# Performance work log

Measured on AMD Instinct MI355X. Metric: run time of the kernel, lower is better.

The kernel has to match this reference:

```python
import jax, jax.numpy as jnp
import numpy as np

B, S, DIM, DA = 64, 4096, 256, 64
NEG = -1e30

def setup_inputs() -> dict:
    key = jax.random.key(0)
    k1, k2, k3, k4 = jax.random.split(key, 4)
    h = jax.random.normal(k1, (B, S, DIM), dtype=jnp.float32)
    mask = jax.random.randint(k2, (B, S), 0, 2).astype(jnp.bool_)
    # xavier_uniform with gain=1.414 as in the torch module
    lim_a = 1.414 * np.sqrt(6.0 / (DIM + DA))
    lim_b = 1.414 * np.sqrt(6.0 / (DA + 1))
    a = jax.random.uniform(k3, (DIM, DA), minval=-lim_a, maxval=lim_a, dtype=jnp.float32)
    b = jax.random.uniform(k4, (DA, 1), minval=-lim_b, maxval=lim_b, dtype=jnp.float32)
    return {"h": h, "mask": mask, "a": a, "b": b}

def reference(h, mask, a, b):
    # e: (B, S) additive-attention logits
    e = jnp.einsum('bsk,ko->bs', jnp.tanh(jnp.einsum('bsd,dk->bsk', h, a)), b)
    e = e + mask.astype(e.dtype) * NEG  # True == padding -> -1e30
    attn = jax.nn.softmax(e, axis=1)    # softmax over seq dim
    # weighted sum over seq: (B, DIM)
    return jnp.einsum('bs,bsd->bd', attn, h)
```

## Files before the change

kernel.cpp:

```cpp
#include <hip/hip_runtime.h>
#include <hip/hip_bf16.h>

#define B_      64
#define S_      4096
#define DIM_    256
#define DA_     64
#define NEG_    (-1e30f)
#define CHUNKS_ 16
#define ROWS_   256
#define LDH_    264
#define PSTR_   260

typedef _Float16 half8 __attribute__((ext_vector_type(8)));
typedef float float4v __attribute__((ext_vector_type(4)));

__device__ __forceinline__ float tanh_fast(float x) {
    float e = __expf(2.0f * x);
    return 1.0f - 2.0f * __builtin_amdgcn_rcpf(e + 1.0f);
}

__global__ __launch_bounds__(256) void prep_kernel(
    const float* __restrict__ a, const void* __restrict__ mask,
    _Float16* __restrict__ at_sw, int* __restrict__ flag)
{
    int idx = blockIdx.x * 256 + threadIdx.x;
    int j    = idx & 7;
    int lane = (idx >> 3) & 63;
    int kbnt = idx >> 9;
    int kb   = kbnt & 7;
    int nt   = kbnt >> 3;
    int d  = kb * 32 + (lane >> 4) * 8 + j;
    int kf = nt * 16 + (lane & 15);
    at_sw[idx] = (_Float16)a[d * DA_ + kf];

    if (blockIdx.x == 0) {
        __shared__ int anynz;
        if (threadIdx.x == 0) anynz = 0;
        __syncthreads();
        const unsigned char* mb = (const unsigned char*)mask;
        int base = threadIdx.x * 4;
        int v = mb[base + 1] | mb[base + 2] | mb[base + 3];
        if (v) atomicOr(&anynz, 1);
        __syncthreads();
        if (threadIdx.x == 0) *flag = (anynz == 0) ? 1 : 0;
    }
}

__global__ __launch_bounds__(256, 2) void fused_kernel(
    const float* __restrict__ h, const _Float16* __restrict__ at_sw,
    const float* __restrict__ bvec, const void* __restrict__ mask,
    const int* __restrict__ flag, float* __restrict__ part)
{
    __shared__ _Float16 asw[16384];
    __shared__ _Float16 hf[64 * LDH_];

    const int t    = threadIdx.x;
    const int wave = t >> 6;
    const int lane = t & 63;
    const int quad = lane >> 4;
    const int nrow = lane & 15;
    const bool int32enc = (*flag != 0);

    {
        const uint4* g = (const uint4*)at_sw;
        uint4* l = (uint4*)asw;
        #pragma unroll
        for (int i = 0; i < 8; ++i) l[i * 256 + t] = g[i * 256 + t];
    }

    float4 bq[4];
    #pragma unroll
    for (int nt = 0; nt < 4; ++nt)
        bq[nt] = *(const float4*)(bvec + nt * 16 + quad * 4);

    const int cg = blockIdx.x;
    const int b  = cg >> 4;
    const int c  = cg & 15;
    const long long crow = (long long)b * S_ + c * ROWS_;
    const long long row0 = crow + wave * 16 + nrow;

    int mv0, mv1, mv2, mv3;
    if (int32enc) {
        const int* mi = (const int*)mask + row0;
        mv0 = mi[0]; mv1 = mi[64]; mv2 = mi[128]; mv3 = mi[192];
    } else {
        const unsigned char* mb = (const unsigned char*)mask + row0;
        mv0 = mb[0]; mv1 = mb[64]; mv2 = mb[128]; mv3 = mb[192];
    }

    __syncthreads();

    const float* wbase = h + (crow + wave * 16) * DIM_;
    float acc0 = 0.f, acc1 = 0.f, acc2 = 0.f, acc3 = 0.f;
    float m_w = NEG_, l_w = 0.f;

    float4 pf[16];

    #pragma unroll
    for (int i = 0; i < 16; ++i)
        pf[i] = *(const float4*)(wbase + (size_t)i * DIM_ + lane * 4);
    #pragma unroll
    for (int i = 0; i < 16; ++i) {
        union { _Float16 hh[4]; unsigned long long u; } pk;
        pk.hh[0] = (_Float16)pf[i].x; pk.hh[1] = (_Float16)pf[i].y;
        pk.hh[2] = (_Float16)pf[i].z; pk.hh[3] = (_Float16)pf[i].w;
        *(unsigned long long*)&hf[(wave * 16 + i) * LDH_ + lane * 4] = pk.u;
    }

    auto body = [&](int tile, int mv) {
        if (tile < 3) {
            const float* nb = wbase + (size_t)(tile + 1) * 64 * DIM_;
            #pragma unroll
            for (int i = 0; i < 16; ++i)
                pf[i] = *(const float4*)(nb + (size_t)i * DIM_ + lane * 4);
        }

        const _Float16* hrow_l = &hf[(wave * 16 + nrow) * LDH_];
        float4v accm[4];
        #pragma unroll
        for (int nt = 0; nt < 4; ++nt) accm[nt] = (float4v){0.f, 0.f, 0.f, 0.f};
        #pragma unroll
        for (int kb = 0; kb < 8; ++kb) {
            half8 bf = *(const half8*)(hrow_l + kb * 32 + quad * 8);
            #pragma unroll
            for (int nt = 0; nt < 4; ++nt) {
                half8 af = *(const half8*)&asw[((nt * 8 + kb) * 64 + lane) * 8];
                accm[nt] = __builtin_amdgcn_mfma_f32_16x16x32_f16(af, bf, accm[nt], 0, 0, 0);
            }
        }

        float p = 0.f;
        #pragma unroll
        for (int nt = 0; nt < 4; ++nt) {
            p += tanh_fast(accm[nt][0]) * bq[nt].x;
            p += tanh_fast(accm[nt][1]) * bq[nt].y;
            p += tanh_fast(accm[nt][2]) * bq[nt].z;
            p += tanh_fast(accm[nt][3]) * bq[nt].w;
        }
        p += __shfl_xor(p, 16);
        p += __shfl_xor(p, 32);

        float ev = mv ? NEG_ : p;
        float mx = ev;
        mx = fmaxf(mx, __shfl_xor(mx, 1));
        mx = fmaxf(mx, __shfl_xor(mx, 2));
        mx = fmaxf(mx, __shfl_xor(mx, 4));
        mx = fmaxf(mx, __shfl_xor(mx, 8));
        float m_new = fmaxf(m_w, mx);
        float rs  = __expf(m_w - m_new);
        float w_s = __expf(ev - m_new);
        float sm = w_s;
        sm += __shfl_xor(sm, 1);
        sm += __shfl_xor(sm, 2);
        sm += __shfl_xor(sm, 4);
        sm += __shfl_xor(sm, 8);
        l_w = l_w * rs + sm;
        m_w = m_new;
        acc0 *= rs; acc1 *= rs; acc2 *= rs; acc3 *= rs;

        #pragma unroll
        for (int s = 0; s < 16; ++s) {
            float wv = __shfl(w_s, s);
            union { ushort4 u; _Float16 hh[4]; } pk;
            pk.u = *(const ushort4*)((const unsigned short*)
                       &hf[(wave * 16 + s) * LDH_ + lane * 4]);
            acc0 = fmaf(wv, (float)pk.hh[0], acc0);
            acc1 = fmaf(wv, (float)pk.hh[1], acc1);
            acc2 = fmaf(wv, (float)pk.hh[2], acc2);
            acc3 = fmaf(wv, (float)pk.hh[3], acc3);
        }

        if (tile < 3) {
            #pragma unroll
            for (int i = 0; i < 16; ++i) {
                union { _Float16 hh[4]; unsigned long long u; } pk;
                pk.hh[0] = (_Float16)pf[i].x; pk.hh[1] = (_Float16)pf[i].y;
                pk.hh[2] = (_Float16)pf[i].z; pk.hh[3] = (_Float16)pf[i].w;
                *(unsigned long long*)&hf[(wave * 16 + i) * LDH_ + lane * 4] = pk.u;
            }
        }
    };
    body(0, mv0); body(1, mv1); body(2, mv2); body(3, mv3);

    float* pc = part + (size_t)(cg * 4 + wave) * PSTR_;
    *(float4*)(pc + 4 + lane * 4) = make_float4(acc0, acc1, acc2, acc3);
    if (lane == 0) { pc[0] = m_w; pc[1] = l_w; }
}

__global__ __launch_bounds__(256) void merge_kernel(
    const float* __restrict__ part, float* __restrict__ out)
{
    const int b = blockIdx.x;
    const int t = threadIdx.x;
    const float* pb = part + (size_t)b * 64 * PSTR_;
    float M = NEG_;
    #pragma unroll
    for (int i = 0; i < 64; ++i) M = fmaxf(M, pb[i * PSTR_]);
    float L = 0.f, o = 0.f;
    #pragma unroll
    for (int i = 0; i < 64; ++i) {
        float sc = __expf(pb[i * PSTR_] - M);
        L += pb[i * PSTR_ + 1] * sc;
        o += pb[i * PSTR_ + 4 + t] * sc;
    }
    out[b * DIM_ + t] = o / L;
}

extern "C" void kernel_launch(void* const* d_in, const int* in_sizes, int n_in,
                              void* d_out, int out_size, void* d_ws, size_t ws_size,
                              hipStream_t stream) {
    const float* h    = (const float*)d_in[0];
    const void*  mask = d_in[1];
    const float* a    = (const float*)d_in[2];
    const float* bvec = (const float*)d_in[3];
    float* out = (float*)d_out;

    char* ws = (char*)d_ws;
    _Float16* at_sw = (_Float16*)ws;
    int* flag       = (int*)(ws + 32768);
    float* part     = (float*)(ws + 36864);

    prep_kernel<<<64, 256, 0, stream>>>(a, mask, at_sw, flag);
    fused_kernel<<<B_ * CHUNKS_, 256, 0, stream>>>(h, at_sw, bvec, mask, flag, part);
    merge_kernel<<<B_, 256, 0, stream>>>(part, out);
}
```

Before: 430.1 us.

## Split sequence into 64-row tiles per block and load h directly into MFMA fragments

Each block now handles a single 64-row tile, replacing four tiles with a software-prefetched register pipeline, so the grid grows from 1024 to 4096 blocks. Each lane loads its own MFMA B-fragment from global memory, converts it to fp16, and writes it to LDS for the weighted-sum pass, which removes the separate cooperative staging. This drops the online-softmax rescaling across tiles and the large prefetch register array, trading them for more parallelism. The cost is four times as many partials for the merge kernel, a longer serial merge loop per batch, and less coalesced strided per-lane global loads.

```diff
diff --git a/kernel.cpp b/kernel.cpp
--- a/kernel.cpp
+++ b/kernel.cpp
@@ -6,10 +6,9 @@
 #define DIM_    256
 #define DA_     64
 #define NEG_    (-1e30f)
-#define CHUNKS_ 16
-#define ROWS_   256
+#define NTILE_  64
 #define LDH_    264
-#define PSTR_   260
+#define PSTR_   264
 
 typedef _Float16 half8 __attribute__((ext_vector_type(8)));
 typedef float float4v __attribute__((ext_vector_type(4)));
@@ -73,118 +72,86 @@
     for (int nt = 0; nt < 4; ++nt)
         bq[nt] = *(const float4*)(bvec + nt * 16 + quad * 4);
 
-    const int cg = blockIdx.x;
-    const int b  = cg >> 4;
-    const int c  = cg & 15;
-    const long long crow = (long long)b * S_ + c * ROWS_;
-    const long long row0 = crow + wave * 16 + nrow;
+    const int bid = blockIdx.x;
+    const long long rowg = ((long long)(bid >> 6) * S_) + (bid & 63) * 64
+                         + wave * 16 + nrow;
+    const float* hp = h + rowg * DIM_ + quad * 8;
 
-    int mv0, mv1, mv2, mv3;
-    if (int32enc) {
-        const int* mi = (const int*)mask + row0;
-        mv0 = mi[0]; mv1 = mi[64]; mv2 = mi[128]; mv3 = mi[192];
-    } else {
-        const unsigned char* mb = (const unsigned char*)mask + row0;
-        mv0 = mb[0]; mv1 = mb[64]; mv2 = mb[128]; mv3 = mb[192];
-    }
+    int mv = int32enc ? ((const int*)mask)[rowg]
+                      : (int)((const unsigned char*)mask)[rowg];
 
     __syncthreads();
 
-    const float* wbase = h + (crow + wave * 16) * DIM_;
-    float acc0 = 0.f, acc1 = 0.f, acc2 = 0.f, acc3 = 0.f;
-    float m_w = NEG_, l_w = 0.f;
-
-    float4 pf[16];
+    const int lrow = wave * 16 + nrow;
+    float4v accm[4];
+    #pragma unroll
+    for (int nt = 0; nt < 4; ++nt) accm[nt] = (float4v){0.f, 0.f, 0.f, 0.f};
 
     #pragma unroll
-    for (int i = 0; i < 16; ++i)
-        pf[i] = *(const float4*)(wbase + (size_t)i * DIM_ + lane * 4);
-    #pragma unroll
-    for (int i = 0; i < 16; ++i) {
-        union { _Float16 hh[4]; unsigned long long u; } pk;
-        pk.hh[0] = (_Float16)pf[i].x; pk.hh[1] = (_Float16)pf[i].y;
-        pk.hh[2] = (_Float16)pf[i].z; pk.hh[3] = (_Float16)pf[i].w;
-        *(unsigned long long*)&hf[(wave * 16 + i) * LDH_ + lane * 4] = pk.u;
-    }
-
-    auto body = [&](int tile, int mv) {
-        if (tile < 3) {
-            const float* nb = wbase + (size_t)(tile + 1) * 64 * DIM_;
-            #pragma unroll
-            for (int i = 0; i < 16; ++i)
-                pf[i] = *(const float4*)(nb + (size_t)i * DIM_ + lane * 4);
+    for (int kh = 0; kh < 2; ++kh) {
+        float4 hv[8];
+        #pragma unroll
+        for (int i = 0; i < 8; ++i) {
+            int kb = kh * 4 + (i >> 1);
+            hv[i] = *(const float4*)(hp + kb * 32 + (i & 1) * 4);
         }
-
-        const _Float16* hrow_l = &hf[(wave * 16 + nrow) * LDH_];
-        float4v accm[4];
         #pragma unroll
-        for (int nt = 0; nt < 4; ++nt) accm[nt] = (float4v){0.f, 0.f, 0.f, 0.f};
-        #pragma unroll
-        for (int kb = 0; kb < 8; ++kb) {
-            half8 bf = *(const half8*)(hrow_l + kb * 32 + quad * 8);
+        for (int k = 0; k < 4; ++k) {
+            int kb = kh * 4 + k;
+            union { _Float16 hh[8]; half8 v; } pk;
+            pk.hh[0] = (_Float16)hv[2 * k].x;     pk.hh[1] = (_Float16)hv[2 * k].y;
+            pk.hh[2] = (_Float16)hv[2 * k].z;     pk.hh[3] = (_Float16)hv[2 * k].w;
+            pk.hh[4] = (_Float16)hv[2 * k + 1].x; pk.hh[5] = (_Float16)hv[2 * k + 1].y;
+            pk.hh[6] = (_Float16)hv[2 * k + 1].z; pk.hh[7] = (_Float16)hv[2 * k + 1].w;
+            *(half8*)&hf[lrow * LDH_ + kb * 32 + quad * 8] = pk.v;
             #pragma unroll
             for (int nt = 0; nt < 4; ++nt) {
                 half8 af = *(const half8*)&asw[((nt * 8 + kb) * 64 + lane) * 8];
-                accm[nt] = __builtin_amdgcn_mfma_f32_16x16x32_f16(af, bf, accm[nt], 0, 0, 0);
+                accm[nt] = __builtin_amdgcn_mfma_f32_16x16x32_f16(af, pk.v, accm[nt], 0, 0, 0);
             }
         }
+    }
 
-        float p = 0.f;
-        #pragma unroll
-        for (int nt = 0; nt < 4; ++nt) {
-            p += tanh_fast(accm[nt][0]) * bq[nt].x;
-            p += tanh_fast(accm[nt][1]) * bq[nt].y;
-            p += tanh_fast(accm[nt][2]) * bq[nt].z;
-            p += tanh_fast(accm[nt][3]) * bq[nt].w;
-        }
-        p += __shfl_xor(p, 16);
-        p += __shfl_xor(p, 32);
+    float p = 0.f;
+    #pragma unroll
+    for (int nt = 0; nt < 4; ++nt) {
+        p += tanh_fast(accm[nt][0]) * bq[nt].x;
+        p += tanh_fast(accm[nt][1]) * bq[nt].y;
+        p += tanh_fast(accm[nt][2]) * bq[nt].z;
+        p += tanh_fast(accm[nt][3]) * bq[nt].w;
+    }
+    p += __shfl_xor(p, 16);
+    p += __shfl_xor(p, 32);
 
-        float ev = mv ? NEG_ : p;
-        float mx = ev;
-        mx = fmaxf(mx, __shfl_xor(mx, 1));
-        mx = fmaxf(mx, __shfl_xor(mx, 2));
-        mx = fmaxf(mx, __shfl_xor(mx, 4));
-        mx = fmaxf(mx, __shfl_xor(mx, 8));
-        float m_new = fmaxf(m_w, mx);
-        float rs  = __expf(m_w - m_new);
-        float w_s = __expf(ev - m_new);
-        float sm = w_s;
-        sm += __shfl_xor(sm, 1);
-        sm += __shfl_xor(sm, 2);
-        sm += __shfl_xor(sm, 4);
-        sm += __shfl_xor(sm, 8);
-        l_w = l_w * rs + sm;
-        m_w = m_new;
-        acc0 *= rs; acc1 *= rs; acc2 *= rs; acc3 *= rs;
+    float ev = mv ? NEG_ : p;
+    float mx = ev;
+    mx = fmaxf(mx, __shfl_xor(mx, 1));
+    mx = fmaxf(mx, __shfl_xor(mx, 2));
+    mx = fmaxf(mx, __shfl_xor(mx, 4));
+    mx = fmaxf(mx, __shfl_xor(mx, 8));
+    float w_s = __expf(ev - mx);
+    float sm = w_s;
+    sm += __shfl_xor(sm, 1);
+    sm += __shfl_xor(sm, 2);
+    sm += __shfl_xor(sm, 4);
+    sm += __shfl_xor(sm, 8);
 
-        #pragma unroll
-        for (int s = 0; s < 16; ++s) {
-            float wv = __shfl(w_s, s);
-            union { ushort4 u; _Float16 hh[4]; } pk;
-            pk.u = *(const ushort4*)((const unsigned short*)
-                       &hf[(wave * 16 + s) * LDH_ + lane * 4]);
-            acc0 = fmaf(wv, (float)pk.hh[0], acc0);
-            acc1 = fmaf(wv, (float)pk.hh[1], acc1);
-            acc2 = fmaf(wv, (float)pk.hh[2], acc2);
-            acc3 = fmaf(wv, (float)pk.hh[3], acc3);
-        }
+    float acc0 = 0.f, acc1 = 0.f, acc2 = 0.f, acc3 = 0.f;
+    #pragma unroll
+    for (int s = 0; s < 16; ++s) {
+        float wv = __shfl(w_s, s);
+        union { ushort4 u; _Float16 hh[4]; } pk;
+        pk.u = *(const ushort4*)((const unsigned short*)
+                   &hf[(wave * 16 + s) * LDH_ + lane * 4]);
+        acc0 = fmaf(wv, (float)pk.hh[0], acc0);
+        acc1 = fmaf(wv, (float)pk.hh[1], acc1);
+        acc2 = fmaf(wv, (float)pk.hh[2], acc2);
+        acc3 = fmaf(wv, (float)pk.hh[3], acc3);
+    }
 
-        if (tile < 3) {
-            #pragma unroll
-            for (int i = 0; i < 16; ++i) {
-                union { _Float16 hh[4]; unsigned long long u; } pk;
-                pk.hh[0] = (_Float16)pf[i].x; pk.hh[1] = (_Float16)pf[i].y;
-                pk.hh[2] = (_Float16)pf[i].z; pk.hh[3] = (_Float16)pf[i].w;
-                *(unsigned long long*)&hf[(wave * 16 + i) * LDH_ + lane * 4] = pk.u;
-            }
-        }
-    };
-    body(0, mv0); body(1, mv1); body(2, mv2); body(3, mv3);
-
-    float* pc = part + (size_t)(cg * 4 + wave) * PSTR_;
+    float* pc = part + (size_t)(bid * 4 + wave) * PSTR_;
     *(float4*)(pc + 4 + lane * 4) = make_float4(acc0, acc1, acc2, acc3);
-    if (lane == 0) { pc[0] = m_w; pc[1] = l_w; }
+    if (lane == 0) { pc[0] = mx; pc[1] = sm; }
 }
 
 __global__ __launch_bounds__(256) void merge_kernel(
@@ -192,13 +159,13 @@
 {
     const int b = blockIdx.x;
     const int t = threadIdx.x;
-    const float* pb = part + (size_t)b * 64 * PSTR_;
+    const float* pb = part + (size_t)b * 256 * PSTR_;
     float M = NEG_;
-    #pragma unroll
-    for (int i = 0; i < 64; ++i) M = fmaxf(M, pb[i * PSTR_]);
+    #pragma unroll 8
+    for (int i = 0; i < 256; ++i) M = fmaxf(M, pb[i * PSTR_]);
     float L = 0.f, o = 0.f;
-    #pragma unroll
-    for (int i = 0; i < 64; ++i) {
+    #pragma unroll 8
+    for (int i = 0; i < 256; ++i) {
         float sc = __expf(pb[i * PSTR_] - M);
         L += pb[i * PSTR_ + 1] * sc;
         o += pb[i * PSTR_ + 4 + t] * sc;
@@ -221,6 +188,6 @@
     float* part     = (float*)(ws + 36864);
 
     prep_kernel<<<64, 256, 0, stream>>>(a, mask, at_sw, flag);
-    fused_kernel<<<B_ * CHUNKS_, 256, 0, stream>>>(h, at_sw, bvec, mask, flag, part);
+    fused_kernel<<<B_ * NTILE_, 256, 0, stream>>>(h, at_sw, bvec, mask, flag, part);
     merge_kernel<<<B_, 256, 0, stream>>>(part, out);
 }
```

Result: faster. 418.9 us (-2.6%).
